# Optimization experiments

Hardware: AMD Instinct MI355X
Metric: run time of the kernel (lower is better)

The kernel has to match this reference:

```python
import jax, jax.numpy as jnp
import numpy as np

COST_CLASS = 1.0
COST_BBOX = 1.0
COST_GIOU = 1.0


def box_cxcywh_to_xyxy(b):
    cx, cy, w, h = jnp.split(b, 4, axis=-1)
    return jnp.concatenate([cx - 0.5 * w, cy - 0.5 * h, cx + 0.5 * w, cy + 0.5 * h], axis=-1)


def generalized_box_iou(b1, b2):
    # b1: [N,4] xyxy, b2: [M,4] xyxy -> [N,M]
    a1 = (b1[:, 2] - b1[:, 0]) * (b1[:, 3] - b1[:, 1])  # [N]
    a2 = (b2[:, 2] - b2[:, 0]) * (b2[:, 3] - b2[:, 1])  # [M]
    lt = jnp.maximum(b1[:, None, :2], b2[None, :, :2])  # [N,M,2]
    rb = jnp.minimum(b1[:, None, 2:], b2[None, :, 2:])
    wh = jnp.clip(rb - lt, 0.0)
    inter = wh[..., 0] * wh[..., 1]
    union = a1[:, None] + a2[None, :] - inter
    iou = inter / union
    lt_e = jnp.minimum(b1[:, None, :2], b2[None, :, :2])
    rb_e = jnp.maximum(b1[:, None, 2:], b2[None, :, 2:])
    wh_e = jnp.clip(rb_e - lt_e, 0.0)
    area = wh_e[..., 0] * wh_e[..., 1]
    return iou - (area - union) / area


def setup_inputs() -> dict:
    key = jax.random.key(0)
    k1, k2, k3, k4, k5 = jax.random.split(key, 5)
    bs, nq, d, total_tgt = 16, 900, 256, 1600
    return {
        "pred_logits": jax.random.normal(k1, (bs, nq, d), dtype=jnp.float32),
        "pred_boxes": jax.random.uniform(k2, (bs, nq, 4), dtype=jnp.float32),
        "tgt_embs": jax.random.normal(k3, (total_tgt, d), dtype=jnp.float32),
        "tgt_bbox": jax.random.uniform(k4, (total_tgt, 4), dtype=jnp.float32),
        "tgt_sizes": jax.random.randint(k5, (bs,), 0, 100, dtype=jnp.int32),  # only used by host-side LSA
    }


def reference(pred_logits, pred_boxes, tgt_embs, tgt_bbox, tgt_sizes):
    # Returns the sigmoid-squashed cost volume C [bs, num_queries, total_tgt];
    # scipy linear_sum_assignment over tgt_sizes splits is a host-side step.
    bs, nq = pred_logits.shape[:2]
    out_prob = pred_logits.reshape(bs * nq, -1)
    out_bbox = pred_boxes.reshape(bs * nq, 4)
    out_prob = out_prob / jnp.linalg.norm(out_prob, axis=-1, keepdims=True)
    cost_class = jax.nn.relu(out_prob @ tgt_embs.T)                    # [N,M]
    cost_bbox = jnp.sum(jnp.abs(out_bbox[:, None, :] - tgt_bbox[None, :, :]), axis=-1)  # L1 cdist
    cost_giou = -generalized_box_iou(box_cxcywh_to_xyxy(out_bbox), box_cxcywh_to_xyxy(tgt_bbox))
    C = COST_BBOX * cost_bbox + COST_CLASS * cost_class + COST_GIOU * cost_giou
    return jax.nn.sigmoid(C.reshape(bs, nq, -1))
```

## Files before the change

### kernel.cpp

```cpp
#include <hip/hip_runtime.h>

#define N_ROWS 14400
#define M_COLS 1600
#define KDIM   256
#define GRID_X 25
#define GRID_Y 113
#define NWG    (GRID_X * GRID_Y)

typedef __attribute__((ext_vector_type(8))) short bf16x8;
typedef __attribute__((ext_vector_type(4))) float f32x4;

__device__ __forceinline__ short f2bf(float x) {
  union { float f; unsigned u; } v; v.f = x;
  unsigned r = v.u + 0x7FFFu + ((v.u >> 16) & 1u);
  return (short)(r >> 16);
}

__device__ __forceinline__ void gload_lds16(const void* g, void* l) {
  __builtin_amdgcn_global_load_lds(
      (const __attribute__((address_space(1))) void*)g,
      (__attribute__((address_space(3))) void*)l, 16, 0, 0);
}

__global__ __launch_bounds__(256) void prep_kernel(
    const float* __restrict__ logits, const float* __restrict__ embs,
    short* __restrict__ probB, short* __restrict__ embB) {
  const int row = blockIdx.x * 4 + (threadIdx.x >> 6);
  const int lane = threadIdx.x & 63;
  if (row < N_ROWS) {
    const float4 x = ((const float4*)(logits + (size_t)row * KDIM))[lane];
    float s = x.x * x.x + x.y * x.y + x.z * x.z + x.w * x.w;
#pragma unroll
    for (int o = 32; o > 0; o >>= 1) s += __shfl_xor(s, o, 64);
    const float scale = __builtin_amdgcn_rsqf(s);
    short4 o4;
    o4.x = f2bf(x.x * scale); o4.y = f2bf(x.y * scale);
    o4.z = f2bf(x.z * scale); o4.w = f2bf(x.w * scale);
    ((short4*)(probB + (size_t)row * KDIM))[lane] = o4;
  } else {
    const int r = row - N_ROWS;
    const float4 x = ((const float4*)(embs + (size_t)r * KDIM))[lane];
    short4 o4;
    o4.x = f2bf(x.x); o4.y = f2bf(x.y); o4.z = f2bf(x.z); o4.w = f2bf(x.w);
    ((short4*)(embB + (size_t)r * KDIM))[lane] = o4;
  }
}

__global__ __launch_bounds__(256) void cost_kernel(
    const short* __restrict__ probB, const short* __restrict__ embB,
    const float* __restrict__ pbox, const float* __restrict__ tbox,
    float* __restrict__ out) {
  __shared__ short As[128 * 64];
  __shared__ short Bs[64 * 64];
  __shared__ f32x4 rowcc[128], rowxy[128];
  __shared__ f32x4 colcc[64],  colxy[64];
  float* const tbuf = (float*)As;

  const int t = threadIdx.x;
  const int lane = t & 63;
  const int wid = t >> 6;
  const int wr = wid >> 1;
  const int wc = wid & 1;

  const int orig = blockIdx.x;
  const int xcd = orig & 7;
  const int rem = orig >> 3;
  const int q = NWG >> 3, r = NWG & 7;
  const int wgid = (xcd < r ? xcd * (q + 1) : r * (q + 1) + (xcd - r) * q) + rem;
  const int bx = wgid % GRID_X;
  const int by = wgid / GRID_X;
  const int rowBase = by * 128;
  const int colBase = bx * 64;

  if (t < 128) {
    const int idx = rowBase + t;
    const int ci = idx < N_ROWS ? idx : N_ROWS - 1;
    const float4 bb = ((const float4*)pbox)[ci];
    rowcc[t] = (f32x4){bb.x, bb.y, bb.z, bb.w};
    rowxy[t] = (f32x4){fmaf(-0.5f, bb.z, bb.x), fmaf(-0.5f, bb.w, bb.y),
                       fmaf(0.5f, bb.z, bb.x), fmaf(0.5f, bb.w, bb.y)};
  } else if (t < 192) {
    const int c = t - 128;
    const float4 bb = ((const float4*)tbox)[colBase + c];
    colcc[c] = (f32x4){bb.x, bb.y, bb.z, bb.w};
    colxy[c] = (f32x4){fmaf(-0.5f, bb.z, bb.x), fmaf(-0.5f, bb.w, bb.y),
                       fmaf(0.5f, bb.z, bb.x), fmaf(0.5f, bb.w, bb.y)};
  }

  f32x4 acc[4][2];
#pragma unroll
  for (int i = 0; i < 4; ++i)
#pragma unroll
    for (int j = 0; j < 2; ++j) acc[i][j] = (f32x4){0.f, 0.f, 0.f, 0.f};

  const int swz = (lane & 7) ^ (lane >> 3);
  const int rbase = wid * 8 + (lane >> 3);

  for (int kt = 0; kt < 4; ++kt) {
    const int k0 = kt * 64 + swz * 8;
#pragma unroll
    for (int i = 0; i < 4; ++i) {
      int gr = rowBase + i * 32 + rbase;
      if (gr > N_ROWS - 1) gr = N_ROWS - 1;
      gload_lds16(probB + (size_t)gr * KDIM + k0, As + (i * 32 + wid * 8) * 64);
    }
#pragma unroll
    for (int i = 0; i < 2; ++i) {
      const int gc = colBase + i * 32 + rbase;
      gload_lds16(embB + (size_t)gc * KDIM + k0, Bs + (i * 32 + wid * 8) * 64);
    }
    __syncthreads();
#pragma unroll
    for (int kk = 0; kk < 2; ++kk) {
      bf16x8 af[4], bfr[2];
      const int g = kk * 4 + (lane >> 4);
#pragma unroll
      for (int mi = 0; mi < 4; ++mi) {
        const int row = wr * 64 + mi * 16 + (lane & 15);
        af[mi] = *(const bf16x8*)(As + row * 64 + ((g ^ (row & 7)) * 8));
      }
#pragma unroll
      for (int ni = 0; ni < 2; ++ni) {
        const int row = wc * 32 + ni * 16 + (lane & 15);
        bfr[ni] = *(const bf16x8*)(Bs + row * 64 + ((g ^ (row & 7)) * 8));
      }
#pragma unroll
      for (int mi = 0; mi < 4; ++mi)
#pragma unroll
        for (int ni = 0; ni < 2; ++ni)
          acc[mi][ni] = __builtin_amdgcn_mfma_f32_16x16x32_bf16(
              af[mi], bfr[ni], acc[mi][ni], 0, 0, 0);
    }
    __syncthreads();
  }

  const float LOG2E = 1.44269504f;
  const int jr = (lane >> 4) * 4;
  const int lc = lane & 15;
  f32x4 c0v[2], c1v[2];
  float cav[2];
#pragma unroll
  for (int ni = 0; ni < 2; ++ni) {
    const int cloc = wc * 32 + ni * 16 + lc;
    c0v[ni] = colcc[cloc];
    c1v[ni] = colxy[cloc];
    cav[ni] = c0v[ni][2] * c0v[ni][3];
  }

#pragma unroll
  for (int mi = 0; mi < 4; ++mi) {
#pragma unroll
    for (int j = 0; j < 4; ++j) {
      const int rloc = wr * 64 + mi * 16 + jr + j;
      const f32x4 r0 = rowcc[rloc];
      const f32x4 r1 = rowxy[rloc];
      const float ra = r0[2] * r0[3];
#pragma unroll
      for (int ni = 0; ni < 2; ++ni) {
        const f32x4 c0 = c0v[ni], c1 = c1v[ni];
        const float cc = fmaxf(acc[mi][ni][j], 0.0f);
        const float l1 = fabsf(r0[0] - c0[0]) + fabsf(r0[1] - c0[1]) +
                         fabsf(r0[2] - c0[2]) + fabsf(r0[3] - c0[3]);
        const float ltx = fmaxf(r1[0], c1[0]);
        const float lty = fmaxf(r1[1], c1[1]);
        const float rbx = fminf(r1[2], c1[2]);
        const float rby = fminf(r1[3], c1[3]);
        const float iw = fmaxf(rbx - ltx, 0.f);
        const float ih = fmaxf(rby - lty, 0.f);
        const float inter = iw * ih;
        const float uni = ra + cav[ni] - inter;
        const float ex = fmaxf(r1[2], c1[2]) - fminf(r1[0], c1[0]);
        const float ey = fmaxf(r1[3], c1[3]) - fminf(r1[1], c1[1]);
        const float earea = ex * ey;
        const float Cv = l1 + cc + 1.0f
                         - inter * __builtin_amdgcn_rcpf(uni)
                         - uni * __builtin_amdgcn_rcpf(earea);
        const float sg = __builtin_amdgcn_rcpf(
            1.0f + __builtin_amdgcn_exp2f(-LOG2E * Cv));
        tbuf[(wr * 16 + jr + j) * 68 + wc * 32 + ni * 16 + lc] = sg;
      }
    }
    __syncthreads();
#pragma unroll
    for (int rr = 0; rr < 2; ++rr) {
      const int rch = rr * 16 + (t >> 4);
      const int c4 = (t & 15) * 4;
      const f32x4 v = *(const f32x4*)(tbuf + rch * 68 + c4);
      const int grow = rowBase + ((rch < 16) ? (mi * 16 + rch)
                                             : (64 + mi * 16 + (rch - 16)));
      if (grow < N_ROWS)
        __builtin_nontemporal_store(
            v, (f32x4*)(out + (size_t)grow * M_COLS + colBase + c4));
    }
    __syncthreads();
  }
}

extern "C" void kernel_launch(void* const* d_in, const int* in_sizes, int n_in,
                              void* d_out, int out_size, void* d_ws, size_t ws_size,
                              hipStream_t stream) {
  const float* logits = (const float*)d_in[0];
  const float* pbox   = (const float*)d_in[1];
  const float* embs   = (const float*)d_in[2];
  const float* tbox   = (const float*)d_in[3];
  float* out = (float*)d_out;

  short* probB = (short*)d_ws;
  short* embB  = probB + (size_t)N_ROWS * KDIM;

  prep_kernel<<<(N_ROWS + M_COLS) / 4, 256, 0, stream>>>(logits, embs, probB, embB);

  cost_kernel<<<NWG, 256, 0, stream>>>(probB, embB, pbox, tbox, out);
}
```

Measured before the change: 49.26 us.

## Use per-wave LDS staging for epilogue stores and merge GIoU reciprocals

The epilogue used to stage the whole block's sigmoid tile in shared memory and needed two block-wide barriers per row group. Now each wave writes to its own double-buffered LDS region and drains it with only a wave-local lgkmcnt wait, so those __syncthreads are gone. The two reciprocals in the GIoU term are also folded into one reciprocal of uni*earea. Risks: the odd 35-float row stride makes the 16-byte LDS reads unaligned, and the combined reciprocal may differ slightly in precision or overflow behaviour.

```diff
diff --git a/kernel.cpp b/kernel.cpp
--- a/kernel.cpp
+++ b/kernel.cpp
@@ -50,17 +50,20 @@
     const short* __restrict__ probB, const short* __restrict__ embB,
     const float* __restrict__ pbox, const float* __restrict__ tbox,
     float* __restrict__ out) {
-  __shared__ short As[128 * 64];
-  __shared__ short Bs[64 * 64];
-  __shared__ f32x4 rowcc[128], rowxy[128];
-  __shared__ f32x4 colcc[64],  colxy[64];
-  float* const tbuf = (float*)As;
+  __shared__ __align__(16) char smem[30720];
+  short* const As = (short*)smem;
+  short* const Bs = (short*)(smem + 16384);
+  f32x4* const rowcc = (f32x4*)(smem + 24576);
+  f32x4* const rowxy = rowcc + 128;
+  f32x4* const colcc = rowxy + 128;
+  f32x4* const colxy = colcc + 64;
 
   const int t = threadIdx.x;
   const int lane = t & 63;
   const int wid = t >> 6;
   const int wr = wid >> 1;
   const int wc = wid & 1;
+  float* const twbuf = (float*)smem + wid * 1120;
 
   const int orig = blockIdx.x;
   const int xcd = orig & 7;
@@ -146,9 +149,12 @@
     c1v[ni] = colxy[cloc];
     cav[ni] = c0v[ni][2] * c0v[ni][3];
   }
+  const int rrow = lane >> 2;
+  const int cg = lane & 3;
 
 #pragma unroll
   for (int mi = 0; mi < 4; ++mi) {
+    float* const tb = twbuf + (mi & 1) * 560;
 #pragma unroll
     for (int j = 0; j < 4; ++j) {
       const int rloc = wr * 64 + mi * 16 + jr + j;
@@ -172,27 +178,24 @@
         const float ex = fmaxf(r1[2], c1[2]) - fminf(r1[0], c1[0]);
         const float ey = fmaxf(r1[3], c1[3]) - fminf(r1[1], c1[1]);
         const float earea = ex * ey;
+        const float num = fmaf(uni, uni, inter * earea);
         const float Cv = l1 + cc + 1.0f
-                         - inter * __builtin_amdgcn_rcpf(uni)
-                         - uni * __builtin_amdgcn_rcpf(earea);
+                         - num * __builtin_amdgcn_rcpf(uni * earea);
         const float sg = __builtin_amdgcn_rcpf(
             1.0f + __builtin_amdgcn_exp2f(-LOG2E * Cv));
-        tbuf[(wr * 16 + jr + j) * 68 + wc * 32 + ni * 16 + lc] = sg;
+        tb[(jr + j) * 35 + ni * 16 + lc] = sg;
       }
     }
-    __syncthreads();
-#pragma unroll
-    for (int rr = 0; rr < 2; ++rr) {
-      const int rch = rr * 16 + (t >> 4);
-      const int c4 = (t & 15) * 4;
-      const f32x4 v = *(const f32x4*)(tbuf + rch * 68 + c4);
-      const int grow = rowBase + ((rch < 16) ? (mi * 16 + rch)
-                                             : (64 + mi * 16 + (rch - 16)));
-      if (grow < N_ROWS)
-        __builtin_nontemporal_store(
-            v, (f32x4*)(out + (size_t)grow * M_COLS + colBase + c4));
-    }
-    __syncthreads();
+    asm volatile("s_waitcnt lgkmcnt(0)" ::: "memory");
+    __builtin_amdgcn_sched_barrier(0);
+    const f32x4 v0 = *(const f32x4*)(tb + rrow * 35 + cg * 8);
+    const f32x4 v1 = *(const f32x4*)(tb + rrow * 35 + cg * 8 + 4);
+    const int grow = rowBase + wr * 64 + mi * 16 + rrow;
+    if (grow < N_ROWS) {
+      float* const dst = out + (size_t)grow * M_COLS + colBase + wc * 32 + cg * 8;
+      __builtin_nontemporal_store(v0, (f32x4*)dst);
+      __builtin_nontemporal_store(v1, (f32x4*)(dst + 4));
+    }
   }
 }
 
```

After: 62.26 us. 26.4% more time.
